# Performance work log

Hardware: AMD Instinct MI355X
Metric: run time of the kernel (lower is better)

The kernel has to match this reference:

```python
import jax, jax.numpy as jnp
import numpy as np

B, T, D = 2, 2048, 1024
H = 16
HD = D // H


def setup_inputs() -> dict:
    key = jax.random.key(0)
    ks = jax.random.split(key, 9)
    s = 1.0 / np.sqrt(D)
    return {
        "x": jax.random.normal(ks[0], (B, T, D), dtype=jnp.float32),
        "Wq": jax.random.normal(ks[1], (D, D), dtype=jnp.float32) * s,
        "bq": jax.random.normal(ks[2], (D,), dtype=jnp.float32) * s,
        "Wk": jax.random.normal(ks[3], (D, D), dtype=jnp.float32) * s,
        "bk": jax.random.normal(ks[4], (D,), dtype=jnp.float32) * s,
        "Wv": jax.random.normal(ks[5], (D, D), dtype=jnp.float32) * s,
        "bv": jax.random.normal(ks[6], (D,), dtype=jnp.float32) * s,
        "Wo": jax.random.normal(ks[7], (D, D), dtype=jnp.float32) * s,
        "bo": jax.random.normal(ks[8], (D,), dtype=jnp.float32) * s,
    }


def reference(x, Wq, bq, Wk, bk, Wv, bv, Wo, bo):
    b, t, d = x.shape
    # projections; torch Linear computes x @ W.T + b
    def proj(W, bias):
        y = jnp.einsum("btd,ed->bte", x, W) + bias
        return y.reshape(b, t, H, HD).transpose(0, 2, 1, 3)  # [B,H,T,HD]
    q = proj(Wq, bq)
    k = proj(Wk, bk)
    v = proj(Wv, bv)
    scores = jnp.einsum("bhqd,bhkd->bhqk", q, k) / np.sqrt(HD)  # [B,H,T,T]
    causal = jnp.triu(jnp.ones((t, t), dtype=bool), k=1)
    scores = jnp.where(causal[None, None], jnp.float32(-1e9), scores)
    attn = jax.nn.softmax(scores, axis=-1)
    out = jnp.einsum("bhqk,bhkd->bhqd", attn, v)  # [B,H,T,HD]
    out = out.transpose(0, 2, 1, 3).reshape(b, t, d)
    return jnp.einsum("btd,ed->bte", out, Wo) + bo
```

## Files before the change

### kernel.cpp

```cpp
#include <hip/hip_runtime.h>


#define DEV __device__ __forceinline__

typedef __attribute__((ext_vector_type(8))) __bf16 bf16x8;
typedef __attribute__((ext_vector_type(4))) float f32x4;

DEV unsigned short f2bf(float f) {
  union { float f; unsigned u; } c;
  c.f = f;
  unsigned u = c.u + 0x7FFFu + ((c.u >> 16) & 1u);
  return (unsigned short)(u >> 16);
}

DEV unsigned cvtpk(float lo, float hi) {
  unsigned r;
  asm("v_cvt_pk_bf16_f32 %0, %1, %2" : "=v"(r) : "v"(lo), "v"(hi));
  return r;
}

DEV void gload16(const unsigned short* g, unsigned short* l) {
  __builtin_amdgcn_global_load_lds(
      (const __attribute__((address_space(1))) unsigned int*)g,
      (__attribute__((address_space(3))) unsigned int*)l, 16, 0, 0);
}

DEV f32x4 mfma16(bf16x8 a, bf16x8 b, f32x4 c) {
  return __builtin_amdgcn_mfma_f32_16x16x32_bf16(a, b, c, 0, 0, 0);
}

__global__ __launch_bounds__(256) void k_cvt_all(
    const float* __restrict__ x, const float* __restrict__ wq,
    const float* __restrict__ wk, const float* __restrict__ wv,
    const float* __restrict__ wo, unsigned short* __restrict__ dst) {
  int i = blockIdx.x * blockDim.x + threadIdx.x;
  const float* s;
  int off;
  if (i < 1048576) {
    s = x; off = i;
  } else {
    int j = i - 1048576;
    int w = j >> 18;
    off = j & 262143;
    s = (w == 0) ? wq : (w == 1) ? wk : (w == 2) ? wv : wo;
  }
  float4 v = reinterpret_cast<const float4*>(s)[off];
  uint2 o;
  o.x = (unsigned)f2bf(v.x) | ((unsigned)f2bf(v.y) << 16);
  o.y = (unsigned)f2bf(v.z) | ((unsigned)f2bf(v.w) << 16);
  reinterpret_cast<uint2*>(dst)[i] = o;
}

DEV void gemm_stage(const unsigned short* __restrict__ A,
                    const unsigned short* __restrict__ W,
                    unsigned short* la, unsigned short* lb,
                    int m0, int n0, int k0, int tid) {
#pragma unroll
  for (int i = 0; i < 2; ++i) {
    const int c = i * 256 + tid;
    const int row = c >> 2;
    const int cb = (c & 3) << 4;
    gload16(A + (m0 + row) * 1024 + k0 + (cb >> 1),
            (unsigned short*)((char*)la + c * 16));
    gload16(W + (n0 + row) * 1024 + k0 + (cb >> 1),
            (unsigned short*)((char*)lb + c * 16));
  }
}

DEV void gemm_core_128(const unsigned short* __restrict__ A,
                       const unsigned short* __restrict__ W,
                       unsigned short (*la)[128 * 32],
                       unsigned short (*lb)[128 * 32],
                       int m0, int n0, f32x4 (&acc)[4][4]) {
  const int tid = threadIdx.x;
  const int lane = tid & 63;
  const int wave = tid >> 6;
  const int wm = (wave >> 1) * 64, wn = (wave & 1) * 64;

  gemm_stage(A, W, la[0], lb[0], m0, n0, 0, tid);
  __syncthreads();

  for (int kt = 0; kt < 32; ++kt) {
    const int cur = kt & 1;
    if (kt + 1 < 32)
      gemm_stage(A, W, la[cur ^ 1], lb[cur ^ 1], m0, n0, (kt + 1) * 32, tid);
    bf16x8 af[4], bfr[4];
#pragma unroll
    for (int m = 0; m < 4; ++m)
      af[m] = *reinterpret_cast<const bf16x8*>(
          &la[cur][(wm + m * 16 + (lane & 15)) * 32 + ((lane >> 4) << 3)]);
#pragma unroll
    for (int n = 0; n < 4; ++n)
      bfr[n] = *reinterpret_cast<const bf16x8*>(
          &lb[cur][(wn + n * 16 + (lane & 15)) * 32 + ((lane >> 4) << 3)]);
#pragma unroll
    for (int m = 0; m < 4; ++m)
#pragma unroll
      for (int n = 0; n < 4; ++n)
        acc[m][n] = mfma16(af[m], bfr[n], acc[m][n]);
    __syncthreads();
  }
}

__global__ __launch_bounds__(256) void k_gemm_qkv(
    const unsigned short* __restrict__ X, const unsigned short* __restrict__ Wq,
    const unsigned short* __restrict__ Wk, const unsigned short* __restrict__ Wv,
    const float* __restrict__ bq, const float* __restrict__ bk,
    const float* __restrict__ bv, unsigned short* __restrict__ Qo,
    unsigned short* __restrict__ Ko, unsigned short* __restrict__ Vo) {
  __shared__ unsigned short la[2][128 * 32], lb[2][128 * 32];
  const int mode = blockIdx.z;
  const unsigned short* W = (mode == 0) ? Wq : (mode == 1) ? Wk : Wv;
  const float* bias = (mode == 0) ? bq : (mode == 1) ? bk : bv;
  const int m0 = blockIdx.y * 128, n0 = blockIdx.x * 128;
  f32x4 acc[4][4] = {};
  gemm_core_128(X, W, la, lb, m0, n0, acc);

  const int lane = threadIdx.x & 63, wave = threadIdx.x >> 6;
  const int wm = (wave >> 1) * 64, wn = (wave & 1) * 64;
#pragma unroll
  for (int m = 0; m < 4; ++m) {
    const int rbase = m0 + wm + m * 16 + ((lane >> 4) << 2);
    const int b = rbase >> 11;
    const int tb = rbase & 2047;
#pragma unroll
    for (int n = 0; n < 4; ++n) {
      const int col = n0 + wn + n * 16 + (lane & 15);
      const float bb = bias[col];
      const int h = col >> 6, hd = col & 63;
      if (mode == 2) {
        unsigned short e0 = f2bf(acc[m][n][0] + bb);
        unsigned short e1 = f2bf(acc[m][n][1] + bb);
        unsigned short e2 = f2bf(acc[m][n][2] + bb);
        unsigned short e3 = f2bf(acc[m][n][3] + bb);
        uint2 pk;
        pk.x = (unsigned)e0 | ((unsigned)e1 << 16);
        pk.y = (unsigned)e2 | ((unsigned)e3 << 16);
        *reinterpret_cast<uint2*>(
            &Vo[(((b << 4) + h) * 64 + hd) * 2048 + tb]) = pk;
      } else {
#pragma unroll
        for (int r = 0; r < 4; ++r) {
          float v = acc[m][n][r] + bb;
          const int t = tb + r;
          if (mode == 0)
            Qo[((((b << 4) + h) * 2048 + t) << 6) + hd] =
                f2bf(v * 0.180336880f);
          else
            Ko[((((b << 4) + h) * 2048 + t) << 6) + hd] = f2bf(v);
        }
      }
    }
  }
}

__global__ __launch_bounds__(256) void k_gemm_out(
    const unsigned short* __restrict__ Ctx, const unsigned short* __restrict__ Wo,
    const float* __restrict__ bo, float* __restrict__ Out) {
  __shared__ unsigned short la[2][128 * 32], lb[2][64 * 32];
  const int tid = threadIdx.x;
  const int lane = tid & 63, wave = tid >> 6;
  const int m0 = blockIdx.y * 128, n0 = blockIdx.x * 64;
  const int wm = (wave >> 1) * 64, wn = (wave & 1) * 32;
  f32x4 acc[4][2] = {};

#pragma unroll
  for (int i = 0; i < 2; ++i) {
    const int c = i * 256 + tid;
    gload16(Ctx + (m0 + (c >> 2)) * 1024 + ((c & 3) << 3),
            (unsigned short*)((char*)la[0] + c * 16));
  }
  gload16(Wo + (n0 + (tid >> 2)) * 1024 + ((tid & 3) << 3),
          (unsigned short*)((char*)lb[0] + tid * 16));
  __syncthreads();

  for (int kt = 0; kt < 32; ++kt) {
    const int cur = kt & 1;
    if (kt + 1 < 32) {
      const int k0 = (kt + 1) * 32;
#pragma unroll
      for (int i = 0; i < 2; ++i) {
        const int c = i * 256 + tid;
        gload16(Ctx + (m0 + (c >> 2)) * 1024 + k0 + ((c & 3) << 3),
                (unsigned short*)((char*)la[cur ^ 1] + c * 16));
      }
      gload16(Wo + (n0 + (tid >> 2)) * 1024 + k0 + ((tid & 3) << 3),
              (unsigned short*)((char*)lb[cur ^ 1] + tid * 16));
    }
    bf16x8 af[4], bfr[2];
#pragma unroll
    for (int m = 0; m < 4; ++m)
      af[m] = *reinterpret_cast<const bf16x8*>(
          &la[cur][(wm + m * 16 + (lane & 15)) * 32 + ((lane >> 4) << 3)]);
#pragma unroll
    for (int n = 0; n < 2; ++n)
      bfr[n] = *reinterpret_cast<const bf16x8*>(
          &lb[cur][(wn + n * 16 + (lane & 15)) * 32 + ((lane >> 4) << 3)]);
#pragma unroll
    for (int m = 0; m < 4; ++m)
#pragma unroll
      for (int n = 0; n < 2; ++n)
        acc[m][n] = mfma16(af[m], bfr[n], acc[m][n]);
    __syncthreads();
  }

#pragma unroll
  for (int m = 0; m < 4; ++m) {
    const int rbase = m0 + wm + m * 16 + ((lane >> 4) << 2);
#pragma unroll
    for (int n = 0; n < 2; ++n) {
      const int col = n0 + wn + n * 16 + (lane & 15);
      const float bb = bo[col];
#pragma unroll
      for (int r = 0; r < 4; ++r)
        Out[(rbase + r) * 1024 + col] = acc[m][n][r] + bb;
    }
  }
}


DEV void attn_stage(const unsigned short* __restrict__ Kb,
                    const unsigned short* __restrict__ Vb,
                    unsigned short* lk, unsigned short* lv, int kv0, int tid) {
#pragma unroll
  for (int i = 0; i < 2; ++i) {
    const int c = i * 256 + tid;
    const int row = c >> 3;
    const int cb = (c & 7) << 4;
    const int scb = cb ^ ((row & 7) << 4);
    gload16(Kb + (kv0 + row) * 64 + (scb >> 1),
            (unsigned short*)((char*)lk + c * 16));
    gload16(Vb + row * 2048 + kv0 + (scb >> 1),
            (unsigned short*)((char*)lv + c * 16));
  }
}

DEV void attn_step(const unsigned short* lk, const unsigned short* lv,
                   unsigned short (&lp)[16][72], const bf16x8 (&qf)[2],
                   f32x4 (&o)[4], float& lsum, int lane, int qloc, bool diag) {
  const int g = lane >> 4;
  f32x4 st[4];
#pragma unroll
  for (int n = 0; n < 4; ++n) {
    f32x4 z = {};
    const int row = n * 16 + (lane & 15);
    const int sw = (row & 7) << 4;
#pragma unroll
    for (int kk = 0; kk < 2; ++kk) {
      bf16x8 kf = *reinterpret_cast<const bf16x8*>(
          (char*)lk + row * 128 + ((kk * 64 + (g << 4)) ^ sw));
      z = mfma16(kf, qf[kk], z);
    }
    st[n] = z;
  }
  if (diag) {
#pragma unroll
    for (int n = 0; n < 4; ++n)
#pragma unroll
      for (int r = 0; r < 4; ++r)
        if (n * 16 + g * 4 + r > qloc) st[n][r] = -1e30f;
  }
  float rs = 0.f;
#pragma unroll
  for (int n = 0; n < 4; ++n)
#pragma unroll
    for (int r = 0; r < 4; ++r) {
      float p = exp2f(st[n][r]);
      st[n][r] = p;
      rs += p;
    }
  lsum += rs;
#pragma unroll
  for (int n = 0; n < 4; ++n) {
    uint2 w;
    w.x = cvtpk(st[n][0], st[n][1]);
    w.y = cvtpk(st[n][2], st[n][3]);
    *reinterpret_cast<uint2*>(&lp[lane & 15][n * 16 + g * 4]) = w;
  }
  asm volatile("s_waitcnt lgkmcnt(0)" ::: "memory");
  __builtin_amdgcn_sched_barrier(0);
  bf16x8 pb[2];
  pb[0] = *reinterpret_cast<const bf16x8*>(&lp[lane & 15][g * 8]);
  pb[1] = *reinterpret_cast<const bf16x8*>(&lp[lane & 15][32 + g * 8]);
#pragma unroll
  for (int h = 0; h < 4; ++h) {
    const int row = h * 16 + (lane & 15);
    const int sw = (row & 7) << 4;
#pragma unroll
    for (int kk = 0; kk < 2; ++kk) {
      bf16x8 vf = *reinterpret_cast<const bf16x8*>(
          (char*)lv + row * 128 + ((kk * 64 + (g << 4)) ^ sw));
      o[h] = mfma16(vf, pb[kk], o[h]);
    }
  }
}

DEV void attn_step_dual(const unsigned short* lk, const unsigned short* lv,
                        unsigned short (&lpA)[16][72],
                        unsigned short (&lpB)[16][72],
                        const bf16x8 (&qfA)[2], const bf16x8 (&qfB)[2],
                        f32x4 (&oA)[4], f32x4 (&oB)[4], float& lsA, float& lsB,
                        int lane, int qloc, bool diagA) {
  const int g = lane >> 4;
  f32x4 sA[4], sB[4];
#pragma unroll
  for (int n = 0; n < 4; ++n) {
    f32x4 zA = {}, zB = {};
    const int row = n * 16 + (lane & 15);
    const int sw = (row & 7) << 4;
#pragma unroll
    for (int kk = 0; kk < 2; ++kk) {
      bf16x8 kf = *reinterpret_cast<const bf16x8*>(
          (char*)lk + row * 128 + ((kk * 64 + (g << 4)) ^ sw));
      zB = mfma16(kf, qfB[kk], zB);
      zA = mfma16(kf, qfA[kk], zA);
    }
    sA[n] = zA;
    sB[n] = zB;
  }
  if (diagA) {
#pragma unroll
    for (int n = 0; n < 4; ++n)
#pragma unroll
      for (int r = 0; r < 4; ++r)
        if (n * 16 + g * 4 + r > qloc) sA[n][r] = -1e30f;
  }
  float rsA = 0.f, rsB = 0.f;
#pragma unroll
  for (int n = 0; n < 4; ++n)
#pragma unroll
    for (int r = 0; r < 4; ++r) {
      float pA = exp2f(sA[n][r]);
      float pB = exp2f(sB[n][r]);
      sA[n][r] = pA;
      sB[n][r] = pB;
      rsA += pA;
      rsB += pB;
    }
  lsA += rsA;
  lsB += rsB;
#pragma unroll
  for (int n = 0; n < 4; ++n) {
    uint2 wA, wB;
    wA.x = cvtpk(sA[n][0], sA[n][1]);
    wA.y = cvtpk(sA[n][2], sA[n][3]);
    wB.x = cvtpk(sB[n][0], sB[n][1]);
    wB.y = cvtpk(sB[n][2], sB[n][3]);
    *reinterpret_cast<uint2*>(&lpA[lane & 15][n * 16 + g * 4]) = wA;
    *reinterpret_cast<uint2*>(&lpB[lane & 15][n * 16 + g * 4]) = wB;
  }
  asm volatile("s_waitcnt lgkmcnt(0)" ::: "memory");
  __builtin_amdgcn_sched_barrier(0);
  bf16x8 pbA[2], pbB[2];
  pbA[0] = *reinterpret_cast<const bf16x8*>(&lpA[lane & 15][g * 8]);
  pbA[1] = *reinterpret_cast<const bf16x8*>(&lpA[lane & 15][32 + g * 8]);
  pbB[0] = *reinterpret_cast<const bf16x8*>(&lpB[lane & 15][g * 8]);
  pbB[1] = *reinterpret_cast<const bf16x8*>(&lpB[lane & 15][32 + g * 8]);
#pragma unroll
  for (int h = 0; h < 4; ++h) {
    const int row = h * 16 + (lane & 15);
    const int sw = (row & 7) << 4;
#pragma unroll
    for (int kk = 0; kk < 2; ++kk) {
      bf16x8 vf = *reinterpret_cast<const bf16x8*>(
          (char*)lv + row * 128 + ((kk * 64 + (g << 4)) ^ sw));
      oB[h] = mfma16(vf, pbB[kk], oB[h]);
      oA[h] = mfma16(vf, pbA[kk], oA[h]);
    }
  }
}

DEV void attn_epi(unsigned short* __restrict__ Ctx,
                  unsigned short (&lp)[16][72], const f32x4 (&o)[4],
                  float lsum, int b, int hh, int qbase, int lane) {
  float lt = lsum;
  lt += __shfl_xor(lt, 16);
  lt += __shfl_xor(lt, 32);
  const float inv = 1.f / lt;
  const int g = lane >> 4;
#pragma unroll
  for (int h = 0; h < 4; ++h) {
    uint2 w;
    w.x = cvtpk(o[h][0] * inv, o[h][1] * inv);
    w.y = cvtpk(o[h][2] * inv, o[h][3] * inv);
    *reinterpret_cast<uint2*>(&lp[lane & 15][h * 16 + g * 4]) = w;
  }
  asm volatile("s_waitcnt lgkmcnt(0)" ::: "memory");
  __builtin_amdgcn_sched_barrier(0);
#pragma unroll
  for (int it = 0; it < 2; ++it) {
    const int q = (lane >> 3) + it * 8;
    const int ck = (lane & 7) * 8;
    uint4 v = *reinterpret_cast<const uint4*>(&lp[q][ck]);
    *reinterpret_cast<uint4*>(
        &Ctx[(b * 2048 + qbase + q) * 1024 + hh * 64 + ck]) = v;
  }
}

__global__ __launch_bounds__(256) void k_attn(
    const unsigned short* __restrict__ Q, const unsigned short* __restrict__ K,
    const unsigned short* __restrict__ Vt, unsigned short* __restrict__ Ctx) {
  __shared__ unsigned short lk[2][64 * 64];
  __shared__ unsigned short lv[2][64 * 64];
  __shared__ unsigned short lp[8][16][72];

  const int tid = threadIdx.x, lane = tid & 63, wave = tid >> 6;
  const int ip = blockIdx.x, bh = blockIdx.y;
  const int qtA = ip;
  const int qtB = 31 - ip;
  const int nt = qtB + 1;

  const unsigned short* Kb = K + bh * 2048 * 64;
  const unsigned short* Vb = Vt + bh * 64 * 2048;

  bf16x8 qfA[2], qfB[2];
  {
    const unsigned short* qr =
        Q + (bh * 2048 + qtA * 64 + wave * 16 + (lane & 15)) * 64 + ((lane >> 4) << 3);
    qfA[0] = *reinterpret_cast<const bf16x8*>(qr);
    qfA[1] = *reinterpret_cast<const bf16x8*>(qr + 32);
    qr = Q + (bh * 2048 + qtB * 64 + wave * 16 + (lane & 15)) * 64 + ((lane >> 4) << 3);
    qfB[0] = *reinterpret_cast<const bf16x8*>(qr);
    qfB[1] = *reinterpret_cast<const bf16x8*>(qr + 32);
  }

  f32x4 oA[4] = {}, oB[4] = {};
  float lA = 0.f, lB = 0.f;
  const int qloc = wave * 16 + (lane & 15);

  attn_stage(Kb, Vb, lk[0], lv[0], 0, tid);
  __syncthreads();

  for (int t = 0; t < nt; ++t) {
    const int cur = t & 1;
    if (t + 1 < nt)
      attn_stage(Kb, Vb, lk[cur ^ 1], lv[cur ^ 1], (t + 1) * 64, tid);
    if (t <= qtA)
      attn_step_dual(lk[cur], lv[cur], lp[wave], lp[wave + 4], qfA, qfB, oA,
                     oB, lA, lB, lane, qloc, t == qtA);
    else
      attn_step(lk[cur], lv[cur], lp[wave + 4], qfB, oB, lB, lane, qloc,
                t == qtB);
    __syncthreads();
  }

  const int b = bh >> 4, hh = bh & 15;
  attn_epi(Ctx, lp[wave], oA, lA, b, hh, qtA * 64 + wave * 16, lane);
  attn_epi(Ctx, lp[wave + 4], oB, lB, b, hh, qtB * 64 + wave * 16, lane);
}

extern "C" void kernel_launch(void* const* d_in, const int* in_sizes, int n_in,
                              void* d_out, int out_size, void* d_ws,
                              size_t ws_size, hipStream_t stream) {
  const float* x = (const float*)d_in[0];
  const float* Wq = (const float*)d_in[1];
  const float* bq = (const float*)d_in[2];
  const float* Wk = (const float*)d_in[3];
  const float* bk = (const float*)d_in[4];
  const float* Wv = (const float*)d_in[5];
  const float* bv = (const float*)d_in[6];
  const float* Wo = (const float*)d_in[7];
  const float* bo = (const float*)d_in[8];
  float* out = (float*)d_out;

  char* ws = (char*)d_ws;
  unsigned short* xb = (unsigned short*)(ws);
  unsigned short* wqb = (unsigned short*)(ws + (8u << 20));
  unsigned short* wkb = (unsigned short*)(ws + (10u << 20));
  unsigned short* wvb = (unsigned short*)(ws + (12u << 20));
  unsigned short* wob = (unsigned short*)(ws + (14u << 20));
  unsigned short* Qb = (unsigned short*)(ws + (16u << 20));
  unsigned short* Kb = (unsigned short*)(ws + (24u << 20));
  unsigned short* Vtb = (unsigned short*)(ws + (32u << 20));
  unsigned short* Ctx = (unsigned short*)(ws + (40u << 20));

  k_cvt_all<<<8192, 256, 0, stream>>>(x, Wq, Wk, Wv, Wo, xb);

  k_gemm_qkv<<<dim3(8, 32, 3), 256, 0, stream>>>(xb, wqb, wkb, wvb, bq, bk, bv,
                                                 Qb, Kb, Vtb);
  k_attn<<<dim3(16, 32), 256, 0, stream>>>(Qb, Kb, Vtb, Ctx);
  k_gemm_out<<<dim3(16, 32), 256, 0, stream>>>(Ctx, wob, bo, out);
}
```

Before: 128.4 us.

## Triple-buffer LDS staging with vmcnt-based waits in GEMMs and attention

Moves the QKV GEMM, the output GEMM and the attention kernel from double buffering to triple buffering of their LDS tiles. Each step now prefetches two tiles ahead and waits with explicit s_waitcnt vmcnt counts plus raw s_barrier, so loads stay in flight across iterations instead of being drained by __syncthreads. The intent is to hide global-memory latency better. In exchange the kernels use more LDS, which may lower occupancy, and the last iterations issue redundant clamped loads of the final tile.

```diff
diff --git a/kernel.cpp b/kernel.cpp
--- a/kernel.cpp
+++ b/kernel.cpp
@@ -28,6 +28,10 @@
 DEV f32x4 mfma16(bf16x8 a, bf16x8 b, f32x4 c) {
   return __builtin_amdgcn_mfma_f32_16x16x32_bf16(a, b, c, 0, 0, 0);
 }
+
+#define WAITVM(n) asm volatile("s_waitcnt vmcnt(" #n ")" ::: "memory")
+#define BAR() __builtin_amdgcn_s_barrier()
+#define SCHEDB() __builtin_amdgcn_sched_barrier(0)
 
 __global__ __launch_bounds__(256) void k_cvt_all(
     const float* __restrict__ x, const float* __restrict__ wq,
@@ -78,27 +82,32 @@
   const int wm = (wave >> 1) * 64, wn = (wave & 1) * 64;
 
   gemm_stage(A, W, la[0], lb[0], m0, n0, 0, tid);
-  __syncthreads();
+  gemm_stage(A, W, la[1], lb[1], m0, n0, 32, tid);
+  WAITVM(4);
+  BAR();
 
   for (int kt = 0; kt < 32; ++kt) {
-    const int cur = kt & 1;
-    if (kt + 1 < 32)
-      gemm_stage(A, W, la[cur ^ 1], lb[cur ^ 1], m0, n0, (kt + 1) * 32, tid);
+    const int nx = (kt + 2 < 32) ? kt + 2 : 31;
+    const int sb = (kt + 2) % 3, cb = kt % 3;
+    gemm_stage(A, W, la[sb], lb[sb], m0, n0, nx * 32, tid);
+    WAITVM(8);
+    BAR();
+    SCHEDB();
     bf16x8 af[4], bfr[4];
 #pragma unroll
     for (int m = 0; m < 4; ++m)
       af[m] = *reinterpret_cast<const bf16x8*>(
-          &la[cur][(wm + m * 16 + (lane & 15)) * 32 + ((lane >> 4) << 3)]);
+          &la[cb][(wm + m * 16 + (lane & 15)) * 32 + ((lane >> 4) << 3)]);
 #pragma unroll
     for (int n = 0; n < 4; ++n)
       bfr[n] = *reinterpret_cast<const bf16x8*>(
-          &lb[cur][(wn + n * 16 + (lane & 15)) * 32 + ((lane >> 4) << 3)]);
+          &lb[cb][(wn + n * 16 + (lane & 15)) * 32 + ((lane >> 4) << 3)]);
 #pragma unroll
     for (int m = 0; m < 4; ++m)
 #pragma unroll
       for (int n = 0; n < 4; ++n)
         acc[m][n] = mfma16(af[m], bfr[n], acc[m][n]);
-    __syncthreads();
+    BAR();
   }
 }
 
@@ -108,7 +117,7 @@
     const float* __restrict__ bq, const float* __restrict__ bk,
     const float* __restrict__ bv, unsigned short* __restrict__ Qo,
     unsigned short* __restrict__ Ko, unsigned short* __restrict__ Vo) {
-  __shared__ unsigned short la[2][128 * 32], lb[2][128 * 32];
+  __shared__ unsigned short la[3][128 * 32], lb[3][128 * 32];
   const int mode = blockIdx.z;
   const unsigned short* W = (mode == 0) ? Wq : (mode == 1) ? Wk : Wv;
   const float* bias = (mode == 0) ? bq : (mode == 1) ? bk : bv;
@@ -157,52 +166,53 @@
 __global__ __launch_bounds__(256) void k_gemm_out(
     const unsigned short* __restrict__ Ctx, const unsigned short* __restrict__ Wo,
     const float* __restrict__ bo, float* __restrict__ Out) {
-  __shared__ unsigned short la[2][128 * 32], lb[2][64 * 32];
+  __shared__ unsigned short la[3][128 * 32], lb[3][64 * 32];
   const int tid = threadIdx.x;
   const int lane = tid & 63, wave = tid >> 6;
   const int m0 = blockIdx.y * 128, n0 = blockIdx.x * 64;
   const int wm = (wave >> 1) * 64, wn = (wave & 1) * 32;
   f32x4 acc[4][2] = {};
 
-#pragma unroll
-  for (int i = 0; i < 2; ++i) {
-    const int c = i * 256 + tid;
-    gload16(Ctx + (m0 + (c >> 2)) * 1024 + ((c & 3) << 3),
-            (unsigned short*)((char*)la[0] + c * 16));
-  }
-  gload16(Wo + (n0 + (tid >> 2)) * 1024 + ((tid & 3) << 3),
-          (unsigned short*)((char*)lb[0] + tid * 16));
-  __syncthreads();
+#define STG_OUT(buf, k0)                                                     \
+  {                                                                          \
+    _Pragma("unroll") for (int i = 0; i < 2; ++i) {                          \
+      const int c = i * 256 + tid;                                           \
+      gload16(Ctx + (m0 + (c >> 2)) * 1024 + (k0) + ((c & 3) << 3),          \
+              (unsigned short*)((char*)la[buf] + c * 16));                   \
+    }                                                                        \
+    gload16(Wo + (n0 + (tid >> 2)) * 1024 + (k0) + ((tid & 3) << 3),         \
+            (unsigned short*)((char*)lb[buf] + tid * 16));                   \
+  }
+
+  STG_OUT(0, 0);
+  STG_OUT(1, 32);
+  WAITVM(3);
+  BAR();
 
   for (int kt = 0; kt < 32; ++kt) {
-    const int cur = kt & 1;
-    if (kt + 1 < 32) {
-      const int k0 = (kt + 1) * 32;
-#pragma unroll
-      for (int i = 0; i < 2; ++i) {
-        const int c = i * 256 + tid;
-        gload16(Ctx + (m0 + (c >> 2)) * 1024 + k0 + ((c & 3) << 3),
-                (unsigned short*)((char*)la[cur ^ 1] + c * 16));
-      }
-      gload16(Wo + (n0 + (tid >> 2)) * 1024 + k0 + ((tid & 3) << 3),
-              (unsigned short*)((char*)lb[cur ^ 1] + tid * 16));
-    }
+    const int nx = (kt + 2 < 32) ? kt + 2 : 31;
+    const int sb = (kt + 2) % 3, cb = kt % 3;
+    STG_OUT(sb, nx * 32);
+    WAITVM(6);
+    BAR();
+    SCHEDB();
     bf16x8 af[4], bfr[2];
 #pragma unroll
     for (int m = 0; m < 4; ++m)
       af[m] = *reinterpret_cast<const bf16x8*>(
-          &la[cur][(wm + m * 16 + (lane & 15)) * 32 + ((lane >> 4) << 3)]);
+          &la[cb][(wm + m * 16 + (lane & 15)) * 32 + ((lane >> 4) << 3)]);
 #pragma unroll
     for (int n = 0; n < 2; ++n)
       bfr[n] = *reinterpret_cast<const bf16x8*>(
-          &lb[cur][(wn + n * 16 + (lane & 15)) * 32 + ((lane >> 4) << 3)]);
+          &lb[cb][(wn + n * 16 + (lane & 15)) * 32 + ((lane >> 4) << 3)]);
 #pragma unroll
     for (int m = 0; m < 4; ++m)
 #pragma unroll
       for (int n = 0; n < 2; ++n)
         acc[m][n] = mfma16(af[m], bfr[n], acc[m][n]);
-    __syncthreads();
-  }
+    BAR();
+  }
+#undef STG_OUT
 
 #pragma unroll
   for (int m = 0; m < 4; ++m) {
@@ -278,7 +288,7 @@
     *reinterpret_cast<uint2*>(&lp[lane & 15][n * 16 + g * 4]) = w;
   }
   asm volatile("s_waitcnt lgkmcnt(0)" ::: "memory");
-  __builtin_amdgcn_sched_barrier(0);
+  SCHEDB();
   bf16x8 pb[2];
   pb[0] = *reinterpret_cast<const bf16x8*>(&lp[lane & 15][g * 8]);
   pb[1] = *reinterpret_cast<const bf16x8*>(&lp[lane & 15][32 + g * 8]);
@@ -350,7 +360,7 @@
     *reinterpret_cast<uint2*>(&lpB[lane & 15][n * 16 + g * 4]) = wB;
   }
   asm volatile("s_waitcnt lgkmcnt(0)" ::: "memory");
-  __builtin_amdgcn_sched_barrier(0);
+  SCHEDB();
   bf16x8 pbA[2], pbB[2];
   pbA[0] = *reinterpret_cast<const bf16x8*>(&lpA[lane & 15][g * 8]);
   pbA[1] = *reinterpret_cast<const bf16x8*>(&lpA[lane & 15][32 + g * 8]);
@@ -386,7 +396,7 @@
     *reinterpret_cast<uint2*>(&lp[lane & 15][h * 16 + g * 4]) = w;
   }
   asm volatile("s_waitcnt lgkmcnt(0)" ::: "memory");
-  __builtin_amdgcn_sched_barrier(0);
+  SCHEDB();
 #pragma unroll
   for (int it = 0; it < 2; ++it) {
     const int q = (lane >> 3) + it * 8;
@@ -400,8 +410,8 @@
 __global__ __launch_bounds__(256) void k_attn(
     const unsigned short* __restrict__ Q, const unsigned short* __restrict__ K,
     const unsigned short* __restrict__ Vt, unsigned short* __restrict__ Ctx) {
-  __shared__ unsigned short lk[2][64 * 64];
-  __shared__ unsigned short lv[2][64 * 64];
+  __shared__ unsigned short lk[3][64 * 64];
+  __shared__ unsigned short lv[3][64 * 64];
   __shared__ unsigned short lp[8][16][72];
 
   const int tid = threadIdx.x, lane = tid & 63, wave = tid >> 6;
@@ -429,19 +439,24 @@
   const int qloc = wave * 16 + (lane & 15);
 
   attn_stage(Kb, Vb, lk[0], lv[0], 0, tid);
-  __syncthreads();
+  attn_stage(Kb, Vb, lk[1], lv[1], 64, tid);
+  WAITVM(4);
+  BAR();
 
   for (int t = 0; t < nt; ++t) {
-    const int cur = t & 1;
-    if (t + 1 < nt)
-      attn_stage(Kb, Vb, lk[cur ^ 1], lv[cur ^ 1], (t + 1) * 64, tid);
+    const int nx = (t + 2 < nt) ? t + 2 : nt - 1;
+    const int sb = (t + 2) % 3, cb = t % 3;
+    attn_stage(Kb, Vb, lk[sb], lv[sb], nx * 64, tid);
+    WAITVM(8);
+    BAR();
+    SCHEDB();
     if (t <= qtA)
-      attn_step_dual(lk[cur], lv[cur], lp[wave], lp[wave + 4], qfA, qfB, oA,
+      attn_step_dual(lk[cb], lv[cb], lp[wave], lp[wave + 4], qfA, qfB, oA,
                      oB, lA, lB, lane, qloc, t == qtA);
     else
-      attn_step(lk[cur], lv[cur], lp[wave + 4], qfB, oB, lB, lane, qloc,
+      attn_step(lk[cb], lv[cb], lp[wave + 4], qfB, oB, lB, lane, qloc,
                 t == qtB);
-    __syncthreads();
+    BAR();
   }
 
   const int b = bh >> 4, hh = bh & 15;
```

Result: slower. 134.9 us (+5.1%).
